# Kernel optimization log

Hardware: AMD Instinct MI355X
Metric: run time of the kernel (lower is better)

Reference implementation:

```python
import jax, jax.numpy as jnp
import numpy as np

H = W = 64      # input_resolution
WS = 8          # window_size
SS = 4          # shift_size
DIM = 96
HEADS = 4
HEAD_DIM = DIM // HEADS
SCALE = HEAD_DIM ** -0.5
N = WS * WS     # tokens per window
EPS = 1e-5


def _rel_pos_index():
    # static (N, N) int index into the (2*WS-1)^2 bias table
    coords = np.stack(np.meshgrid(np.arange(WS), np.arange(WS), indexing='ij'))  # (2, WS, WS)
    cf = coords.reshape(2, -1)                       # (2, N)
    rel = (cf[:, :, None] - cf[:, None, :]).transpose(1, 2, 0)  # (N, N, 2)
    rel[:, :, 0] += WS - 1
    rel[:, :, 1] += WS - 1
    rel[:, :, 0] *= 2 * WS - 1
    return rel.sum(-1)                               # (N, N)


def _attn_mask():
    # static (nW, N, N) 0/-100 mask for shifted windows
    img = np.zeros((H, W))
    cnt = 0
    sl = (slice(0, -WS), slice(-WS, -SS), slice(-SS, None))
    for hs in sl:
        for ws_ in sl:
            img[hs, ws_] = cnt
            cnt += 1
    mw = img.reshape(H // WS, WS, W // WS, WS).transpose(0, 2, 1, 3).reshape(-1, N)
    diff = mw[:, None, :] - mw[:, :, None]
    return np.where(diff != 0, -100.0, 0.0).astype(np.float32)


_RPI = jnp.asarray(_rel_pos_index())
_MASK = jnp.asarray(_attn_mask())  # (nW, N, N)


def _layernorm(x, g, b):
    mu = jnp.mean(x, axis=-1, keepdims=True)
    var = jnp.mean(jnp.square(x - mu), axis=-1, keepdims=True)
    return (x - mu) * jax.lax.rsqrt(var + EPS) * g + b


def setup_inputs() -> dict:
    key = jax.random.key(0)
    ks = jax.random.split(key, 8)
    s = 0.02
    return {
        'x': jax.random.normal(ks[0], (64, H * W, DIM), jnp.float32),
        'norm1_g': jnp.ones((DIM,), jnp.float32),
        'norm1_b': jnp.zeros((DIM,), jnp.float32),
        'qkv_w': jax.random.normal(ks[1], (3 * DIM, DIM), jnp.float32) * s,
        'qkv_b': jnp.zeros((3 * DIM,), jnp.float32),
        'rel_bias_table': jax.random.normal(ks[2], ((2 * WS - 1) ** 2, HEADS), jnp.float32) * s,
        'proj_w': jax.random.normal(ks[3], (DIM, DIM), jnp.float32) * s,
        'proj_b': jnp.zeros((DIM,), jnp.float32),
        'norm2_g': jnp.ones((DIM,), jnp.float32),
        'norm2_b': jnp.zeros((DIM,), jnp.float32),
        'fc1_w': jax.random.normal(ks[4], (4 * DIM, DIM), jnp.float32) * s,
        'fc1_b': jnp.zeros((4 * DIM,), jnp.float32),
        'fc2_w': jax.random.normal(ks[5], (DIM, 4 * DIM), jnp.float32) * s,
        'fc2_b': jnp.zeros((DIM,), jnp.float32),
    }


def reference(x, norm1_g, norm1_b, qkv_w, qkv_b, rel_bias_table, proj_w, proj_b,
              norm2_g, norm2_b, fc1_w, fc1_b, fc2_w, fc2_b):
    B, L, C = x.shape
    nW = (H // WS) * (W // WS)
    shortcut = x

    h = _layernorm(x, norm1_g, norm1_b).reshape(B, H, W, C)
    h = jnp.roll(h, (-SS, -SS), axis=(1, 2))
    # window partition -> (B*nW, N, C)
    h = h.reshape(B, H // WS, WS, W // WS, WS, C).transpose(0, 1, 3, 2, 4, 5)
    h = h.reshape(B * nW, N, C)

    qkv = h @ qkv_w.T + qkv_b                                   # (B_, N, 3C)
    qkv = qkv.reshape(B * nW, N, 3, HEADS, HEAD_DIM).transpose(2, 0, 3, 1, 4)
    q, k, v = qkv[0] * SCALE, qkv[1], qkv[2]                    # (B_, heads, N, hd)

    attn = jnp.einsum('whnd,whmd->whnm', q, k)                  # (B_, heads, N, N)
    bias = rel_bias_table[_RPI.reshape(-1)].reshape(N, N, HEADS).transpose(2, 0, 1)
    attn = attn + bias[None]
    attn = attn.reshape(B, nW, HEADS, N, N) + _MASK[None, :, None]
    attn = jax.nn.softmax(attn.reshape(B * nW, HEADS, N, N), axis=-1)

    out = jnp.einsum('whnm,whmd->whnd', attn, v)                # (B_, heads, N, hd)
    out = out.transpose(0, 2, 1, 3).reshape(B * nW, N, C)
    out = out @ proj_w.T + proj_b

    # window reverse + un-shift
    out = out.reshape(B, H // WS, W // WS, WS, WS, C).transpose(0, 1, 3, 2, 4, 5)
    out = out.reshape(B, H, W, C)
    out = jnp.roll(out, (SS, SS), axis=(1, 2)).reshape(B, L, C)

    x = shortcut + out
    h2 = _layernorm(x, norm2_g, norm2_b)
    h2 = jax.nn.gelu(h2 @ fc1_w.T + fc1_b, approximate=False)
    h2 = h2 @ fc2_w.T + fc2_b
    return x + h2
```

## Files before the change

kernel.cpp:

```cpp
#include <hip/hip_runtime.h>
#include <hip/hip_fp16.h>
#include <math.h>

typedef _Float16 half_t;
typedef _Float16 half8 __attribute__((ext_vector_type(8)));
typedef _Float16 half4 __attribute__((ext_vector_type(4)));
typedef float f32x4 __attribute__((ext_vector_type(4)));

#define MFMA(a, b, c) __builtin_amdgcn_mfma_f32_16x16x32_f16((a), (b), (c), 0, 0, 0)

static constexpr float kScale = 0.2041241452319315f;
static constexpr int QSTR = 200;
static constexpr int VTS  = 72;
static constexpr int PS   = 72;

__global__ __launch_bounds__(256) void k_convert(const float* __restrict__ qkv_w,
                                                 const float* __restrict__ proj_w,
                                                 const float* __restrict__ fc1_w,
                                                 const float* __restrict__ fc2_w,
                                                 half_t* __restrict__ wbuf) {
  int i = blockIdx.x * 256 + threadIdx.x;
  if (i < 27648)       wbuf[i] = (half_t)qkv_w[i];
  else if (i < 36864)  wbuf[i] = (half_t)proj_w[i - 27648];
  else if (i < 73728)  wbuf[i] = (half_t)fc1_w[i - 36864];
  else                 wbuf[i] = (half_t)fc2_w[i - 73728];
}

__global__ __launch_bounds__(256, 2) void k_attn_fused(
    const float* __restrict__ x, const float* __restrict__ n1g, const float* __restrict__ n1b,
    const half_t* __restrict__ qkvw, const float* __restrict__ qkv_b,
    const float* __restrict__ bias_table, const half_t* __restrict__ projw,
    const float* __restrict__ proj_b, float* __restrict__ out) {
  __shared__ __attribute__((aligned(16))) unsigned char smem[61760];
  half_t* qbuf = (half_t*)smem;
  half_t* vT   = (half_t*)(smem + 25600);
  half_t* pbuf = (half_t*)(smem + 39424);
  float*  tblf = (float*)(smem + 57856);
  int*    regb = (int*)(smem + 61504);

  int tid = threadIdx.x;
  int wave = tid >> 6, lane = tid & 63;
  int l15 = lane & 15, quad = lane >> 4;
  int blk = blockIdx.x;
  int bb = blk >> 6, wh = (blk >> 3) & 7, ww = blk & 7;

  for (int i = tid; i < 900; i += 256) tblf[(i & 3) * 228 + (i >> 2)] = bias_table[i];
  if (tid < 64) {
    int ih = tid >> 3, iw = tid & 7;
    int rr = wh * 8 + ih, cc = ww * 8 + iw;
    regb[tid] = ((rr < 56) ? 0 : ((rr < 60) ? 1 : 2)) * 3 + ((cc < 56) ? 0 : ((cc < 60) ? 1 : 2));
  }

  half8 af[4][3];
  {
    float gg[24], bv[24];
#pragma unroll
    for (int kt = 0; kt < 3; ++kt) {
      int c0 = kt * 32 + quad * 8;
      float4 g0 = *(const float4*)(n1g + c0);
      float4 g1 = *(const float4*)(n1g + c0 + 4);
      float4 b0 = *(const float4*)(n1b + c0);
      float4 b1 = *(const float4*)(n1b + c0 + 4);
      gg[kt*8+0]=g0.x; gg[kt*8+1]=g0.y; gg[kt*8+2]=g0.z; gg[kt*8+3]=g0.w;
      gg[kt*8+4]=g1.x; gg[kt*8+5]=g1.y; gg[kt*8+6]=g1.z; gg[kt*8+7]=g1.w;
      bv[kt*8+0]=b0.x; bv[kt*8+1]=b0.y; bv[kt*8+2]=b0.z; bv[kt*8+3]=b0.w;
      bv[kt*8+4]=b1.x; bv[kt*8+5]=b1.y; bv[kt*8+6]=b1.z; bv[kt*8+7]=b1.w;
    }
#pragma unroll
    for (int g = 0; g < 4; ++g) {
      int tok = g * 16 + l15;
      int sr = (wh * 8 + (tok >> 3) + 4) & 63;
      int sc = (ww * 8 + (tok & 7) + 4) & 63;
      const float* rp = x + ((size_t)bb * 4096 + sr * 64 + sc) * 96;
      float v[24];
      float s1 = 0.f, s2 = 0.f;
#pragma unroll
      for (int kt = 0; kt < 3; ++kt) {
        float4 a = *(const float4*)(rp + kt * 32 + quad * 8);
        float4 b = *(const float4*)(rp + kt * 32 + quad * 8 + 4);
        v[kt*8+0]=a.x; v[kt*8+1]=a.y; v[kt*8+2]=a.z; v[kt*8+3]=a.w;
        v[kt*8+4]=b.x; v[kt*8+5]=b.y; v[kt*8+6]=b.z; v[kt*8+7]=b.w;
      }
#pragma unroll
      for (int c = 0; c < 24; ++c) { s1 += v[c]; s2 += v[c] * v[c]; }
      s1 += __shfl_xor(s1, 16); s1 += __shfl_xor(s1, 32);
      s2 += __shfl_xor(s2, 16); s2 += __shfl_xor(s2, 32);
      float mu = s1 * (1.f / 96.f);
      float inv = rsqrtf(fmaxf(s2 * (1.f / 96.f) - mu * mu, 0.f) + 1e-5f);
#pragma unroll
      for (int kt = 0; kt < 3; ++kt) {
        half8 h;
#pragma unroll
        for (int j = 0; j < 8; ++j)
          h[j] = (half_t)((v[kt*8+j] - mu) * inv * gg[kt*8+j] + bv[kt*8+j]);
        af[g][kt] = h;
      }
    }
  }

  for (int t = wave; t < 18; t += 4) {
    half8 bf[3];
#pragma unroll
    for (int kt = 0; kt < 3; ++kt)
      bf[kt] = *(const half8*)(qkvw + (size_t)(t * 16 + l15) * 96 + kt * 32 + quad * 8);
    f32x4 acc[4] = {{0,0,0,0},{0,0,0,0},{0,0,0,0},{0,0,0,0}};
#pragma unroll
    for (int kt = 0; kt < 3; ++kt)
#pragma unroll
      for (int g = 0; g < 4; ++g)
        acc[g] = MFMA(af[g][kt], bf[kt], acc[g]);
    int col = t * 16 + l15;
    float bias = qkv_b[col];
    if (t < 12) {
      float sc_ = (t < 6) ? kScale : 1.f;
#pragma unroll
      for (int g = 0; g < 4; ++g)
#pragma unroll
        for (int r = 0; r < 4; ++r)
          qbuf[(g * 16 + quad * 4 + r) * QSTR + col] = (half_t)((acc[g][r] + bias) * sc_);
    } else {
      int vc = col - 192;
      int hd = vc / 24, c = vc - hd * 24;
#pragma unroll
      for (int g = 0; g < 4; ++g)
#pragma unroll
        for (int r = 0; r < 4; ++r)
          vT[hd * 24 * VTS + c * VTS + g * 16 + quad * 4 + r] = (half_t)(acc[g][r] + bias);
    }
  }
  __syncthreads();

  {
    int head = wave;
    const half8 z8 = {};
    half8 qa[4], kb[4], vb[2][2];
#pragma unroll
    for (int g = 0; g < 4; ++g) {
      half8 t = *(const half8*)(&qbuf[(g * 16 + l15) * QSTR + head * 24 + quad * 8]);
      qa[g] = (quad < 3) ? t : z8;
    }
#pragma unroll
    for (int nt = 0; nt < 4; ++nt) {
      half8 t = *(const half8*)(&qbuf[(nt * 16 + l15) * QSTR + 96 + head * 24 + quad * 8]);
      kb[nt] = (quad < 3) ? t : z8;
    }
#pragma unroll
    for (int nt = 0; nt < 2; ++nt)
#pragma unroll
      for (int kt = 0; kt < 2; ++kt)
        vb[nt][kt] = *(const half8*)(&vT[head * 24 * VTS + (nt * 16 + l15) * VTS + kt * 32 + quad * 8]);

    float s[4][4][4];
#pragma unroll
    for (int g = 0; g < 4; ++g)
#pragma unroll
      for (int nt = 0; nt < 4; ++nt) {
        f32x4 a = {0, 0, 0, 0};
        a = MFMA(qa[g], kb[nt], a);
#pragma unroll
        for (int r = 0; r < 4; ++r) s[g][nt][r] = a[r];
      }

    int rj[4], jh_[4], jw_[4];
#pragma unroll
    for (int nt = 0; nt < 4; ++nt) {
      int j = nt * 16 + l15;
      rj[nt] = regb[j]; jh_[nt] = j >> 3; jw_[nt] = j & 7;
    }
    float inv_[4][4];
#pragma unroll
    for (int g = 0; g < 4; ++g)
#pragma unroll
      for (int r = 0; r < 4; ++r) {
        int i = g * 16 + quad * 4 + r;
        int ih = i >> 3, iw = i & 7;
        int ri = regb[i];
#pragma unroll
        for (int nt = 0; nt < 4; ++nt) {
          float val = s[g][nt][r] + tblf[head * 228 + (ih - jh_[nt] + 7) * 15 + (iw - jw_[nt] + 7)];
          if (ri != rj[nt]) val -= 100.f;
          s[g][nt][r] = val;
        }
        float mx = fmaxf(fmaxf(s[g][0][r], s[g][1][r]), fmaxf(s[g][2][r], s[g][3][r]));
        mx = fmaxf(mx, __shfl_xor(mx, 1));
        mx = fmaxf(mx, __shfl_xor(mx, 2));
        mx = fmaxf(mx, __shfl_xor(mx, 4));
        mx = fmaxf(mx, __shfl_xor(mx, 8));
        float sum = 0.f;
#pragma unroll
        for (int nt = 0; nt < 4; ++nt) {
          float e = __expf(s[g][nt][r] - mx);
          s[g][nt][r] = e;
          sum += e;
        }
        sum += __shfl_xor(sum, 1);
        sum += __shfl_xor(sum, 2);
        sum += __shfl_xor(sum, 4);
        sum += __shfl_xor(sum, 8);
        inv_[g][r] = 1.f / sum;
      }

    half_t* pb = pbuf + head * 32 * PS;
#pragma unroll
    for (int hv = 0; hv < 2; ++hv) {
#pragma unroll
      for (int g2 = 0; g2 < 2; ++g2) {
        int g = hv * 2 + g2;
#pragma unroll
        for (int nt = 0; nt < 4; ++nt)
#pragma unroll
          for (int r = 0; r < 4; ++r)
            pb[(g2 * 16 + quad * 4 + r) * PS + nt * 16 + l15] = (half_t)s[g][nt][r];
      }
      f32x4 oacc[2][2] = {{{0,0,0,0},{0,0,0,0}},{{0,0,0,0},{0,0,0,0}}};
#pragma unroll
      for (int g2 = 0; g2 < 2; ++g2) {
        half8 pa[2];
#pragma unroll
        for (int kt = 0; kt < 2; ++kt)
          pa[kt] = *(const half8*)(&pb[(g2 * 16 + l15) * PS + kt * 32 + quad * 8]);
#pragma unroll
        for (int nt = 0; nt < 2; ++nt)
#pragma unroll
          for (int kt = 0; kt < 2; ++kt)
            oacc[g2][nt] = MFMA(pa[kt], vb[nt][kt], oacc[g2][nt]);
      }
#pragma unroll
      for (int g2 = 0; g2 < 2; ++g2)
#pragma unroll
        for (int nt = 0; nt < 2; ++nt)
#pragma unroll
          for (int r = 0; r < 4; ++r) {
            int c = nt * 16 + l15;
            if (c < 24)
              qbuf[(hv * 32 + g2 * 16 + quad * 4 + r) * QSTR + head * 24 + c] =
                  (half_t)(oacc[g2][nt][r] * inv_[hv * 2 + g2][r]);
          }
    }
  }
  __syncthreads();

  {
    half8 pa2[4][3];
#pragma unroll
    for (int g = 0; g < 4; ++g)
#pragma unroll
      for (int kt = 0; kt < 3; ++kt)
        pa2[g][kt] = *(const half8*)(&qbuf[(g * 16 + l15) * QSTR + kt * 32 + quad * 8]);
    for (int t = wave; t < 6; t += 4) {
      half8 bf[3];
#pragma unroll
      for (int kt = 0; kt < 3; ++kt)
        bf[kt] = *(const half8*)(projw + (size_t)(t * 16 + l15) * 96 + kt * 32 + quad * 8);
      f32x4 acc[4] = {{0,0,0,0},{0,0,0,0},{0,0,0,0},{0,0,0,0}};
#pragma unroll
      for (int kt = 0; kt < 3; ++kt)
#pragma unroll
        for (int g = 0; g < 4; ++g)
          acc[g] = MFMA(pa2[g][kt], bf[kt], acc[g]);
      int col = t * 16 + l15;
      float bias = proj_b[col];
#pragma unroll
      for (int g = 0; g < 4; ++g)
#pragma unroll
        for (int r = 0; r < 4; ++r) {
          int tok = g * 16 + quad * 4 + r;
          int sr = (wh * 8 + (tok >> 3) + 4) & 63;
          int sc = (ww * 8 + (tok & 7) + 4) & 63;
          size_t fidx = ((size_t)bb * 4096 + sr * 64 + sc) * 96 + col;
          out[fidx] = x[fidx] + acc[g][r] + bias;
        }
    }
  }
}

__global__ __launch_bounds__(512, 4) void k_mlp(
    const float* __restrict__ n2g, const float* __restrict__ n2b,
    const half_t* __restrict__ fc1w, const float* __restrict__ fc1b,
    const half_t* __restrict__ fc2w, const float* __restrict__ fc2b,
    float* __restrict__ out) {
  __shared__ __attribute__((aligned(16))) half_t xn[64 * 104];
  __shared__ __attribute__((aligned(16))) half_t h1[64 * 392];
  int tid = threadIdx.x;
  int wave = tid >> 6, lane = tid & 63;
  int l15 = lane & 15, quad = lane >> 4;
  int rowbase = blockIdx.x * 64;

  {
    int r = wave * 8 + (lane >> 3);
    int ch = lane & 7;
    const float* rp = out + (size_t)(rowbase + r) * 96 + ch * 12;
    float v[12];
    float4 a = *(const float4*)rp;
    float4 b = *(const float4*)(rp + 4);
    float4 c = *(const float4*)(rp + 8);
    v[0]=a.x; v[1]=a.y; v[2]=a.z; v[3]=a.w;
    v[4]=b.x; v[5]=b.y; v[6]=b.z; v[7]=b.w;
    v[8]=c.x; v[9]=c.y; v[10]=c.z; v[11]=c.w;
    float s1 = 0.f, s2 = 0.f;
#pragma unroll
    for (int j = 0; j < 12; ++j) { s1 += v[j]; s2 += v[j] * v[j]; }
    s1 += __shfl_xor(s1, 1); s1 += __shfl_xor(s1, 2); s1 += __shfl_xor(s1, 4);
    s2 += __shfl_xor(s2, 1); s2 += __shfl_xor(s2, 2); s2 += __shfl_xor(s2, 4);
    float mu = s1 * (1.f / 96.f);
    float inv = rsqrtf(fmaxf(s2 * (1.f / 96.f) - mu * mu, 0.f) + 1e-5f);
    float4 g0 = *(const float4*)(n2g + ch * 12);
    float4 g1 = *(const float4*)(n2g + ch * 12 + 4);
    float4 g2 = *(const float4*)(n2g + ch * 12 + 8);
    float4 b0 = *(const float4*)(n2b + ch * 12);
    float4 b1 = *(const float4*)(n2b + ch * 12 + 4);
    float4 b2 = *(const float4*)(n2b + ch * 12 + 8);
    float gv[12] = {g0.x,g0.y,g0.z,g0.w,g1.x,g1.y,g1.z,g1.w,g2.x,g2.y,g2.z,g2.w};
    float bb[12] = {b0.x,b0.y,b0.z,b0.w,b1.x,b1.y,b1.z,b1.w,b2.x,b2.y,b2.z,b2.w};
    half_t* op = xn + r * 104 + ch * 12;
    half4 h0, h1v, h2v;
#pragma unroll
    for (int j = 0; j < 4; ++j) {
      h0[j]  = (half_t)((v[j]     - mu) * inv * gv[j]     + bb[j]);
      h1v[j] = (half_t)((v[j + 4] - mu) * inv * gv[j + 4] + bb[j + 4]);
      h2v[j] = (half_t)((v[j + 8] - mu) * inv * gv[j + 8] + bb[j + 8]);
    }
    *(half4*)(op) = h0; *(half4*)(op + 4) = h1v; *(half4*)(op + 8) = h2v;
  }
  __syncthreads();

  {
    half8 af[4][3];
#pragma unroll
    for (int g = 0; g < 4; ++g)
#pragma unroll
      for (int kt = 0; kt < 3; ++kt)
        af[g][kt] = *(const half8*)(&xn[(g * 16 + l15) * 104 + kt * 32 + quad * 8]);
#pragma unroll
    for (int i = 0; i < 3; ++i) {
      int t = wave * 3 + i;
      int n0 = t * 16 + l15;
      half8 bf[3];
#pragma unroll
      for (int kt = 0; kt < 3; ++kt)
        bf[kt] = *(const half8*)(fc1w + (size_t)n0 * 96 + kt * 32 + quad * 8);
      f32x4 acc[4] = {{0,0,0,0},{0,0,0,0},{0,0,0,0},{0,0,0,0}};
#pragma unroll
      for (int kt = 0; kt < 3; ++kt)
#pragma unroll
        for (int g = 0; g < 4; ++g)
          acc[g] = MFMA(af[g][kt], bf[kt], acc[g]);
      float bias = fc1b[n0];
#pragma unroll
      for (int g = 0; g < 4; ++g)
#pragma unroll
        for (int r = 0; r < 4; ++r) {
          float vv = acc[g][r] + bias;
          vv = 0.5f * vv * (1.f + erff(vv * 0.70710678118f));
          h1[(g * 16 + quad * 4 + r) * 392 + n0] = (half_t)vv;
        }
    }
  }
  __syncthreads();

  {
    int rt = wave >> 1, chh = wave & 1;
    half8 a2[12];
#pragma unroll
    for (int kt = 0; kt < 12; ++kt)
      a2[kt] = *(const half8*)(&h1[(rt * 16 + l15) * 392 + kt * 32 + quad * 8]);
#pragma unroll
    for (int i = 0; i < 3; ++i) {
      int t = chh * 3 + i;
      f32x4 acc = {0, 0, 0, 0};
#pragma unroll
      for (int kt = 0; kt < 12; ++kt) {
        half8 bf = *(const half8*)(fc2w + (size_t)(t * 16 + l15) * 384 + kt * 32 + quad * 8);
        acc = MFMA(a2[kt], bf, acc);
      }
      int col = t * 16 + l15;
      float bias = fc2b[col];
#pragma unroll
      for (int r = 0; r < 4; ++r) {
        size_t o = (size_t)(rowbase + rt * 16 + quad * 4 + r) * 96 + col;
        out[o] += acc[r] + bias;
      }
    }
  }
}

extern "C" void kernel_launch(void* const* d_in, const int* in_sizes, int n_in,
                              void* d_out, int out_size, void* d_ws, size_t ws_size,
                              hipStream_t stream) {
  const float* x      = (const float*)d_in[0];
  const float* n1g    = (const float*)d_in[1];
  const float* n1b    = (const float*)d_in[2];
  const float* qkv_w  = (const float*)d_in[3];
  const float* qkv_b  = (const float*)d_in[4];
  const float* rtbl   = (const float*)d_in[5];
  const float* proj_w = (const float*)d_in[6];
  const float* proj_b = (const float*)d_in[7];
  const float* n2g    = (const float*)d_in[8];
  const float* n2b    = (const float*)d_in[9];
  const float* fc1_w  = (const float*)d_in[10];
  const float* fc1_b  = (const float*)d_in[11];
  const float* fc2_w  = (const float*)d_in[12];
  const float* fc2_b  = (const float*)d_in[13];
  float* out = (float*)d_out;

  if (ws_size < 221184) return;
  half_t* wbuf = (half_t*)d_ws;

  k_convert<<<432, 256, 0, stream>>>(qkv_w, proj_w, fc1_w, fc2_w, wbuf);
  k_attn_fused<<<4096, 256, 0, stream>>>(x, n1g, n1b, wbuf, qkv_b, rtbl,
                                         wbuf + 27648, proj_b, out);
  k_mlp<<<4096, 512, 0, stream>>>(n2g, n2b, wbuf + 36864, fc1_b,
                                  wbuf + 73728, fc2_b, out);
}
```

Before: 491.8 us.

## Fuse attention and MLP kernels into one per-window Swin block kernel

Merges the attention kernel and the MLP kernel into a single kernel in which each block processes one shifted window end to end. The residual after attention is kept in shared memory as fp16 instead of being written to and re-read from global memory, and the MLP works on window-ordered tokens. This removes one kernel launch and a full global round trip of the intermediate activation. In exchange it uses more shared memory per block (76.8KB, with the buffers aliased), runs the MLP with 256 threads instead of 512, and rounds the residual stream to fp16, which may reduce accuracy.

New measurement: 473.9 us. 1.04x faster.

```diff
diff --git a/kernel.cpp b/kernel.cpp
--- a/kernel.cpp
+++ b/kernel.cpp
@@ -4,15 +4,16 @@
 
 typedef _Float16 half_t;
 typedef _Float16 half8 __attribute__((ext_vector_type(8)));
-typedef _Float16 half4 __attribute__((ext_vector_type(4)));
 typedef float f32x4 __attribute__((ext_vector_type(4)));
 
 #define MFMA(a, b, c) __builtin_amdgcn_mfma_f32_16x16x32_f16((a), (b), (c), 0, 0, 0)
 
 static constexpr float kScale = 0.2041241452319315f;
+static constexpr int RS   = 104;
 static constexpr int QSTR = 200;
 static constexpr int VTS  = 72;
 static constexpr int PS   = 72;
+static constexpr int H1S  = 392;
 
 __global__ __launch_bounds__(256) void k_convert(const float* __restrict__ qkv_w,
                                                  const float* __restrict__ proj_w,
@@ -26,17 +27,27 @@
   else                 wbuf[i] = (half_t)fc2_w[i - 73728];
 }
 
-__global__ __launch_bounds__(256, 2) void k_attn_fused(
-    const float* __restrict__ x, const float* __restrict__ n1g, const float* __restrict__ n1b,
+__global__ __launch_bounds__(256, 2) void k_swin(
+    const float* __restrict__ x,
+    const float* __restrict__ n1g, const float* __restrict__ n1b,
     const half_t* __restrict__ qkvw, const float* __restrict__ qkv_b,
-    const float* __restrict__ bias_table, const half_t* __restrict__ projw,
-    const float* __restrict__ proj_b, float* __restrict__ out) {
-  __shared__ __attribute__((aligned(16))) unsigned char smem[61760];
-  half_t* qbuf = (half_t*)smem;
-  half_t* vT   = (half_t*)(smem + 25600);
-  half_t* pbuf = (half_t*)(smem + 39424);
-  float*  tblf = (float*)(smem + 57856);
-  int*    regb = (int*)(smem + 61504);
+    const float* __restrict__ tbl_g, const half_t* __restrict__ projw,
+    const float* __restrict__ proj_b,
+    const float* __restrict__ n2g, const float* __restrict__ n2b,
+    const half_t* __restrict__ fc1w, const float* __restrict__ fc1b,
+    const half_t* __restrict__ fc2w, const float* __restrict__ fc2b,
+    float* __restrict__ out) {
+  __shared__ __attribute__((aligned(16))) unsigned char smem[76800];
+  half_t* resid = (half_t*)smem;
+  unsigned char* U = smem + 13312;
+  half_t* qbuf = (half_t*)U;
+  half_t* vT   = (half_t*)(U + 25600);
+  half_t* pbuf = (half_t*)(U + 39424);
+  half_t* hn   = (half_t*)(U + 39424);
+  float*  tblf = (float*)(U + 57856);
+  int*    regb = (int*)(U + 61504);
+  half_t* h1   = (half_t*)U;
+  half_t* xn   = (half_t*)(U + 50176);
 
   int tid = threadIdx.x;
   int wave = tid >> 6, lane = tid & 63;
@@ -44,15 +55,15 @@
   int blk = blockIdx.x;
   int bb = blk >> 6, wh = (blk >> 3) & 7, ww = blk & 7;
 
-  for (int i = tid; i < 900; i += 256) tblf[(i & 3) * 228 + (i >> 2)] = bias_table[i];
+  for (int i = tid; i < 900; i += 256) tblf[(i & 3) * 228 + (i >> 2)] = tbl_g[i];
   if (tid < 64) {
     int ih = tid >> 3, iw = tid & 7;
     int rr = wh * 8 + ih, cc = ww * 8 + iw;
     regb[tid] = ((rr < 56) ? 0 : ((rr < 60) ? 1 : 2)) * 3 + ((cc < 56) ? 0 : ((cc < 60) ? 1 : 2));
   }
 
-  half8 af[4][3];
-  {
+  {
+    int tok = wave * 16 + l15;
     float gg[24], bv[24];
 #pragma unroll
     for (int kt = 0; kt < 3; ++kt) {
@@ -66,70 +77,81 @@
       bv[kt*8+0]=b0.x; bv[kt*8+1]=b0.y; bv[kt*8+2]=b0.z; bv[kt*8+3]=b0.w;
       bv[kt*8+4]=b1.x; bv[kt*8+5]=b1.y; bv[kt*8+6]=b1.z; bv[kt*8+7]=b1.w;
     }
-#pragma unroll
-    for (int g = 0; g < 4; ++g) {
-      int tok = g * 16 + l15;
-      int sr = (wh * 8 + (tok >> 3) + 4) & 63;
-      int sc = (ww * 8 + (tok & 7) + 4) & 63;
-      const float* rp = x + ((size_t)bb * 4096 + sr * 64 + sc) * 96;
-      float v[24];
-      float s1 = 0.f, s2 = 0.f;
-#pragma unroll
-      for (int kt = 0; kt < 3; ++kt) {
-        float4 a = *(const float4*)(rp + kt * 32 + quad * 8);
-        float4 b = *(const float4*)(rp + kt * 32 + quad * 8 + 4);
-        v[kt*8+0]=a.x; v[kt*8+1]=a.y; v[kt*8+2]=a.z; v[kt*8+3]=a.w;
-        v[kt*8+4]=b.x; v[kt*8+5]=b.y; v[kt*8+6]=b.z; v[kt*8+7]=b.w;
-      }
-#pragma unroll
-      for (int c = 0; c < 24; ++c) { s1 += v[c]; s2 += v[c] * v[c]; }
-      s1 += __shfl_xor(s1, 16); s1 += __shfl_xor(s1, 32);
-      s2 += __shfl_xor(s2, 16); s2 += __shfl_xor(s2, 32);
-      float mu = s1 * (1.f / 96.f);
-      float inv = rsqrtf(fmaxf(s2 * (1.f / 96.f) - mu * mu, 0.f) + 1e-5f);
-#pragma unroll
-      for (int kt = 0; kt < 3; ++kt) {
-        half8 h;
-#pragma unroll
-        for (int j = 0; j < 8; ++j)
-          h[j] = (half_t)((v[kt*8+j] - mu) * inv * gg[kt*8+j] + bv[kt*8+j]);
-        af[g][kt] = h;
-      }
-    }
-  }
-
-  for (int t = wave; t < 18; t += 4) {
-    half8 bf[3];
-#pragma unroll
-    for (int kt = 0; kt < 3; ++kt)
-      bf[kt] = *(const half8*)(qkvw + (size_t)(t * 16 + l15) * 96 + kt * 32 + quad * 8);
-    f32x4 acc[4] = {{0,0,0,0},{0,0,0,0},{0,0,0,0},{0,0,0,0}};
-#pragma unroll
-    for (int kt = 0; kt < 3; ++kt)
-#pragma unroll
-      for (int g = 0; g < 4; ++g)
-        acc[g] = MFMA(af[g][kt], bf[kt], acc[g]);
-    int col = t * 16 + l15;
-    float bias = qkv_b[col];
-    if (t < 12) {
-      float sc_ = (t < 6) ? kScale : 1.f;
-#pragma unroll
-      for (int g = 0; g < 4; ++g)
-#pragma unroll
-        for (int r = 0; r < 4; ++r)
-          qbuf[(g * 16 + quad * 4 + r) * QSTR + col] = (half_t)((acc[g][r] + bias) * sc_);
-    } else {
-      int vc = col - 192;
-      int hd = vc / 24, c = vc - hd * 24;
-#pragma unroll
-      for (int g = 0; g < 4; ++g)
-#pragma unroll
-        for (int r = 0; r < 4; ++r)
-          vT[hd * 24 * VTS + c * VTS + g * 16 + quad * 4 + r] = (half_t)(acc[g][r] + bias);
-    }
-  }
-  __syncthreads();
-
+    int sr = (wh * 8 + (tok >> 3) + 4) & 63;
+    int sc = (ww * 8 + (tok & 7) + 4) & 63;
+    const float* rp = x + ((size_t)bb * 4096 + sr * 64 + sc) * 96;
+    float v[24];
+    float s1 = 0.f, s2 = 0.f;
+#pragma unroll
+    for (int kt = 0; kt < 3; ++kt) {
+      float4 a = *(const float4*)(rp + kt * 32 + quad * 8);
+      float4 b = *(const float4*)(rp + kt * 32 + quad * 8 + 4);
+      v[kt*8+0]=a.x; v[kt*8+1]=a.y; v[kt*8+2]=a.z; v[kt*8+3]=a.w;
+      v[kt*8+4]=b.x; v[kt*8+5]=b.y; v[kt*8+6]=b.z; v[kt*8+7]=b.w;
+    }
+#pragma unroll
+    for (int c = 0; c < 24; ++c) { s1 += v[c]; s2 += v[c] * v[c]; }
+    s1 += __shfl_xor(s1, 16); s1 += __shfl_xor(s1, 32);
+    s2 += __shfl_xor(s2, 16); s2 += __shfl_xor(s2, 32);
+    float mu = s1 * (1.f / 96.f);
+    float inv = rsqrtf(fmaxf(s2 * (1.f / 96.f) - mu * mu, 0.f) + 1e-5f);
+#pragma unroll
+    for (int kt = 0; kt < 3; ++kt) {
+      half8 hh, rr;
+#pragma unroll
+      for (int j = 0; j < 8; ++j) {
+        float val = v[kt*8+j];
+        rr[j] = (half_t)val;
+        hh[j] = (half_t)((val - mu) * inv * gg[kt*8+j] + bv[kt*8+j]);
+      }
+      *(half8*)(&resid[tok * RS + kt * 32 + quad * 8]) = rr;
+      *(half8*)(&hn[tok * RS + kt * 32 + quad * 8]) = hh;
+    }
+  }
+  __syncthreads();
+
+  {
+    half8 af[4][3];
+#pragma unroll
+    for (int g = 0; g < 4; ++g)
+#pragma unroll
+      for (int kt = 0; kt < 3; ++kt)
+        af[g][kt] = *(const half8*)(&hn[(g * 16 + l15) * RS + kt * 32 + quad * 8]);
+    for (int t = wave; t < 18; t += 4) {
+      half8 bf[3];
+#pragma unroll
+      for (int kt = 0; kt < 3; ++kt)
+        bf[kt] = *(const half8*)(qkvw + (size_t)(t * 16 + l15) * 96 + kt * 32 + quad * 8);
+      f32x4 acc[4] = {{0,0,0,0},{0,0,0,0},{0,0,0,0},{0,0,0,0}};
+#pragma unroll
+      for (int kt = 0; kt < 3; ++kt)
+#pragma unroll
+        for (int g = 0; g < 4; ++g)
+          acc[g] = MFMA(af[g][kt], bf[kt], acc[g]);
+      int col = t * 16 + l15;
+      float bias = qkv_b[col];
+      if (t < 12) {
+        float sc_ = (t < 6) ? kScale : 1.f;
+#pragma unroll
+        for (int g = 0; g < 4; ++g)
+#pragma unroll
+          for (int r = 0; r < 4; ++r)
+            qbuf[(g * 16 + quad * 4 + r) * QSTR + col] = (half_t)((acc[g][r] + bias) * sc_);
+      } else {
+        int vc = col - 192;
+        int hd = vc / 24, c = vc - hd * 24;
+#pragma unroll
+        for (int g = 0; g < 4; ++g)
+#pragma unroll
+          for (int r = 0; r < 4; ++r)
+            vT[hd * 24 * VTS + c * VTS + g * 16 + quad * 4 + r] = (half_t)(acc[g][r] + bias);
+      }
+    }
+  }
+  __syncthreads();
+
+  f32x4 oacc[2][2][2];
+  float inv_[4][4];
   {
     int head = wave;
     const half8 z8 = {};
@@ -167,7 +189,6 @@
       int j = nt * 16 + l15;
       rj[nt] = regb[j]; jh_[nt] = j >> 3; jw_[nt] = j & 7;
     }
-    float inv_[4][4];
 #pragma unroll
     for (int g = 0; g < 4; ++g)
 #pragma unroll
@@ -212,7 +233,6 @@
           for (int r = 0; r < 4; ++r)
             pb[(g2 * 16 + quad * 4 + r) * PS + nt * 16 + l15] = (half_t)s[g][nt][r];
       }
-      f32x4 oacc[2][2] = {{{0,0,0,0},{0,0,0,0}},{{0,0,0,0},{0,0,0,0}}};
 #pragma unroll
       for (int g2 = 0; g2 < 2; ++g2) {
         half8 pa[2];
@@ -220,11 +240,20 @@
         for (int kt = 0; kt < 2; ++kt)
           pa[kt] = *(const half8*)(&pb[(g2 * 16 + l15) * PS + kt * 32 + quad * 8]);
 #pragma unroll
-        for (int nt = 0; nt < 2; ++nt)
-#pragma unroll
-          for (int kt = 0; kt < 2; ++kt)
-            oacc[g2][nt] = MFMA(pa[kt], vb[nt][kt], oacc[g2][nt]);
-      }
+        for (int nt = 0; nt < 2; ++nt) {
+          f32x4 a = {0, 0, 0, 0};
+#pragma unroll
+          for (int kt = 0; kt < 2; ++kt) a = MFMA(pa[kt], vb[nt][kt], a);
+          oacc[hv][g2][nt] = a;
+        }
+      }
+    }
+  }
+  __syncthreads();
+  {
+    int head = wave;
+#pragma unroll
+    for (int hv = 0; hv < 2; ++hv)
 #pragma unroll
       for (int g2 = 0; g2 < 2; ++g2)
 #pragma unroll
@@ -234,9 +263,8 @@
             int c = nt * 16 + l15;
             if (c < 24)
               qbuf[(hv * 32 + g2 * 16 + quad * 4 + r) * QSTR + head * 24 + c] =
-                  (half_t)(oacc[g2][nt][r] * inv_[hv * 2 + g2][r]);
+                  (half_t)(oacc[hv][g2][nt][r] * inv_[hv * 2 + g2][r]);
           }
-    }
   }
   __syncthreads();
 
@@ -264,76 +292,61 @@
       for (int g = 0; g < 4; ++g)
 #pragma unroll
         for (int r = 0; r < 4; ++r) {
-          int tok = g * 16 + quad * 4 + r;
-          int sr = (wh * 8 + (tok >> 3) + 4) & 63;
-          int sc = (ww * 8 + (tok & 7) + 4) & 63;
-          size_t fidx = ((size_t)bb * 4096 + sr * 64 + sc) * 96 + col;
-          out[fidx] = x[fidx] + acc[g][r] + bias;
+          int row = g * 16 + quad * 4 + r;
+          float rv = (float)resid[row * RS + col] + acc[g][r] + bias;
+          resid[row * RS + col] = (half_t)rv;
         }
     }
   }
-}
-
-__global__ __launch_bounds__(512, 4) void k_mlp(
-    const float* __restrict__ n2g, const float* __restrict__ n2b,
-    const half_t* __restrict__ fc1w, const float* __restrict__ fc1b,
-    const half_t* __restrict__ fc2w, const float* __restrict__ fc2b,
-    float* __restrict__ out) {
-  __shared__ __attribute__((aligned(16))) half_t xn[64 * 104];
-  __shared__ __attribute__((aligned(16))) half_t h1[64 * 392];
-  int tid = threadIdx.x;
-  int wave = tid >> 6, lane = tid & 63;
-  int l15 = lane & 15, quad = lane >> 4;
-  int rowbase = blockIdx.x * 64;
-
-  {
-    int r = wave * 8 + (lane >> 3);
-    int ch = lane & 7;
-    const float* rp = out + (size_t)(rowbase + r) * 96 + ch * 12;
-    float v[12];
-    float4 a = *(const float4*)rp;
-    float4 b = *(const float4*)(rp + 4);
-    float4 c = *(const float4*)(rp + 8);
-    v[0]=a.x; v[1]=a.y; v[2]=a.z; v[3]=a.w;
-    v[4]=b.x; v[5]=b.y; v[6]=b.z; v[7]=b.w;
-    v[8]=c.x; v[9]=c.y; v[10]=c.z; v[11]=c.w;
+  __syncthreads();
+
+  {
+    int r4 = wave * 16 + (lane >> 2);
+    int ch = lane & 3;
+    const half_t* rp = resid + r4 * RS + ch * 24;
+    half8 w0 = *(const half8*)(rp);
+    half8 w1 = *(const half8*)(rp + 8);
+    half8 w2 = *(const half8*)(rp + 16);
+    float v[24];
+#pragma unroll
+    for (int j = 0; j < 8; ++j) {
+      v[j] = (float)w0[j]; v[j + 8] = (float)w1[j]; v[j + 16] = (float)w2[j];
+    }
     float s1 = 0.f, s2 = 0.f;
 #pragma unroll
-    for (int j = 0; j < 12; ++j) { s1 += v[j]; s2 += v[j] * v[j]; }
-    s1 += __shfl_xor(s1, 1); s1 += __shfl_xor(s1, 2); s1 += __shfl_xor(s1, 4);
-    s2 += __shfl_xor(s2, 1); s2 += __shfl_xor(s2, 2); s2 += __shfl_xor(s2, 4);
+    for (int j = 0; j < 24; ++j) { s1 += v[j]; s2 += v[j] * v[j]; }
+    s1 += __shfl_xor(s1, 1); s1 += __shfl_xor(s1, 2);
+    s2 += __shfl_xor(s2, 1); s2 += __shfl_xor(s2, 2);
     float mu = s1 * (1.f / 96.f);
     float inv = rsqrtf(fmaxf(s2 * (1.f / 96.f) - mu * mu, 0.f) + 1e-5f);
-    float4 g0 = *(const float4*)(n2g + ch * 12);
-    float4 g1 = *(const float4*)(n2g + ch * 12 + 4);
-    float4 g2 = *(const float4*)(n2g + ch * 12 + 8);
-    float4 b0 = *(const float4*)(n2b + ch * 12);
-    float4 b1 = *(const float4*)(n2b + ch * 12 + 4);
-    float4 b2 = *(const float4*)(n2b + ch * 12 + 8);
-    float gv[12] = {g0.x,g0.y,g0.z,g0.w,g1.x,g1.y,g1.z,g1.w,g2.x,g2.y,g2.z,g2.w};
-    float bb[12] = {b0.x,b0.y,b0.z,b0.w,b1.x,b1.y,b1.z,b1.w,b2.x,b2.y,b2.z,b2.w};
-    half_t* op = xn + r * 104 + ch * 12;
-    half4 h0, h1v, h2v;
-#pragma unroll
-    for (int j = 0; j < 4; ++j) {
-      h0[j]  = (half_t)((v[j]     - mu) * inv * gv[j]     + bb[j]);
-      h1v[j] = (half_t)((v[j + 4] - mu) * inv * gv[j + 4] + bb[j + 4]);
-      h2v[j] = (half_t)((v[j + 8] - mu) * inv * gv[j + 8] + bb[j + 8]);
-    }
-    *(half4*)(op) = h0; *(half4*)(op + 4) = h1v; *(half4*)(op + 8) = h2v;
-  }
-  __syncthreads();
-
-  {
-    half8 af[4][3];
+    float gv[24], bb2[24];
+#pragma unroll
+    for (int q = 0; q < 6; ++q) {
+      float4 g4 = *(const float4*)(n2g + ch * 24 + q * 4);
+      float4 b4 = *(const float4*)(n2b + ch * 24 + q * 4);
+      gv[q*4+0]=g4.x; gv[q*4+1]=g4.y; gv[q*4+2]=g4.z; gv[q*4+3]=g4.w;
+      bb2[q*4+0]=b4.x; bb2[q*4+1]=b4.y; bb2[q*4+2]=b4.z; bb2[q*4+3]=b4.w;
+    }
+    half_t* op = xn + r4 * RS + ch * 24;
+#pragma unroll
+    for (int q = 0; q < 3; ++q) {
+      half8 h;
+#pragma unroll
+      for (int j = 0; j < 8; ++j)
+        h[j] = (half_t)((v[q*8+j] - mu) * inv * gv[q*8+j] + bb2[q*8+j]);
+      *(half8*)(op + q * 8) = h;
+    }
+  }
+  __syncthreads();
+
+  {
+    half8 a5[4][3];
 #pragma unroll
     for (int g = 0; g < 4; ++g)
 #pragma unroll
       for (int kt = 0; kt < 3; ++kt)
-        af[g][kt] = *(const half8*)(&xn[(g * 16 + l15) * 104 + kt * 32 + quad * 8]);
-#pragma unroll
-    for (int i = 0; i < 3; ++i) {
-      int t = wave * 3 + i;
+        a5[g][kt] = *(const half8*)(&xn[(g * 16 + l15) * RS + kt * 32 + quad * 8]);
+    for (int t = wave; t < 24; t += 4) {
       int n0 = t * 16 + l15;
       half8 bf[3];
 #pragma unroll
@@ -344,7 +357,7 @@
       for (int kt = 0; kt < 3; ++kt)
 #pragma unroll
         for (int g = 0; g < 4; ++g)
-          acc[g] = MFMA(af[g][kt], bf[kt], acc[g]);
+          acc[g] = MFMA(a5[g][kt], bf[kt], acc[g]);
       float bias = fc1b[n0];
 #pragma unroll
       for (int g = 0; g < 4; ++g)
@@ -352,21 +365,20 @@
         for (int r = 0; r < 4; ++r) {
           float vv = acc[g][r] + bias;
           vv = 0.5f * vv * (1.f + erff(vv * 0.70710678118f));
-          h1[(g * 16 + quad * 4 + r) * 392 + n0] = (half_t)vv;
+          h1[(g * 16 + quad * 4 + r) * H1S + n0] = (half_t)vv;
         }
     }
   }
   __syncthreads();
 
   {
-    int rt = wave >> 1, chh = wave & 1;
+    int rt = wave;
     half8 a2[12];
 #pragma unroll
     for (int kt = 0; kt < 12; ++kt)
-      a2[kt] = *(const half8*)(&h1[(rt * 16 + l15) * 392 + kt * 32 + quad * 8]);
-#pragma unroll
-    for (int i = 0; i < 3; ++i) {
-      int t = chh * 3 + i;
+      a2[kt] = *(const half8*)(&h1[(rt * 16 + l15) * H1S + kt * 32 + quad * 8]);
+#pragma unroll
+    for (int t = 0; t < 6; ++t) {
       f32x4 acc = {0, 0, 0, 0};
 #pragma unroll
       for (int kt = 0; kt < 12; ++kt) {
@@ -377,8 +389,11 @@
       float bias = fc2b[col];
 #pragma unroll
       for (int r = 0; r < 4; ++r) {
-        size_t o = (size_t)(rowbase + rt * 16 + quad * 4 + r) * 96 + col;
-        out[o] += acc[r] + bias;
+        int tok = rt * 16 + quad * 4 + r;
+        int sr = (wh * 8 + (tok >> 3) + 4) & 63;
+        int sc = (ww * 8 + (tok & 7) + 4) & 63;
+        size_t fidx = ((size_t)bb * 4096 + sr * 64 + sc) * 96 + col;
+        out[fidx] = (float)resid[tok * RS + col] + acc[r] + bias;
       }
     }
   }
@@ -407,8 +422,7 @@
   half_t* wbuf = (half_t*)d_ws;
 
   k_convert<<<432, 256, 0, stream>>>(qkv_w, proj_w, fc1_w, fc2_w, wbuf);
-  k_attn_fused<<<4096, 256, 0, stream>>>(x, n1g, n1b, wbuf, qkv_b, rtbl,
-                                         wbuf + 27648, proj_b, out);
-  k_mlp<<<4096, 512, 0, stream>>>(n2g, n2b, wbuf + 36864, fc1_b,
-                                  wbuf + 73728, fc2_b, out);
+  k_swin<<<4096, 256, 0, stream>>>(x, n1g, n1b, wbuf, qkv_b, rtbl,
+                                   wbuf + 27648, proj_b, n2g, n2b,
+                                   wbuf + 36864, fc1_b, wbuf + 73728, fc2_b, out);
 }
```
